# Kernel tuning notes

Measured on AMD Instinct MI355X. Metric: run time of the kernel, lower is better.

## Reference

```python
import jax, jax.numpy as jnp
import numpy as np

# dims
T, INPUT_DIM = 128, 512
C_INT, ISQ, DIM, C = 8, 16, 256, 8  # internal_channels, input_square_dim, dim, n_channel
OSQ, OUT_CH = 8, 16                  # output_square_dim, output_size // osq^2
INPUT_SCALE, S1, S2 = 1.0, 0.9, 0.1
K1, D1, K2, D2 = 3, 1, 5, 2


def dw_circ_conv(x, w, dilation):
    """Depthwise conv with circular padding. x: [B,C,H,W], w: [C,1,k,k]."""
    k = w.shape[-1]
    pad = dilation * (k - 1) // 2
    xp = jnp.pad(x, ((0, 0), (0, 0), (pad, pad), (pad, pad)), mode='wrap')
    return jax.lax.conv_general_dilated(
        xp, w, window_strides=(1, 1), padding='VALID',
        rhs_dilation=(dilation, dilation), feature_group_count=x.shape[1])


def setup_inputs() -> dict:
    key = jax.random.key(0)
    ks = jax.random.split(key, 10)
    X = jax.random.normal(ks[0], (T, INPUT_DIM), jnp.float32)
    # nn.Linear weight [out, in]
    W_embed = jax.random.normal(ks[1], (C_INT * ISQ * ISQ, INPUT_DIM), jnp.float32) * 0.02
    mask_coarse = jax.random.bernoulli(ks[2], 0.5, (1, 1, ISQ, ISQ)).astype(jnp.float32)
    mask_fine = jax.random.bernoulli(ks[3], 0.5, (1, 1, DIM, DIM)).astype(jnp.float32)
    # ConvTranspose2d weight [in_ch, out_ch, k, k], k = dim // isq = 16
    W_deconv = jax.random.normal(ks[4], (C_INT, C, DIM // ISQ, DIM // ISQ), jnp.float32) * 0.02

    def lateral_w(k, ksz, p):
        # LateralConnections with conn_exp=1: |w| * bernoulli(p), normalized per output channel
        w = jnp.abs(jax.random.normal(k, (C, 1, ksz, ksz), jnp.float32))
        m = jax.random.bernoulli(jax.random.fold_in(k, 1), p, w.shape).astype(jnp.float32)
        w = w * m
        return w / w.sum(axis=(1, 2, 3), keepdims=True)

    w1 = lateral_w(ks[5], K1, 0.9)
    w2 = lateral_w(ks[6], K2, 0.9)
    # output Conv2d: [out_ch, in_ch, k, k], k = dim // osq = 32
    w_out = jax.random.normal(ks[7], (OUT_CH, C, DIM // OSQ, DIM // OSQ), jnp.float32) * 0.01
    b_out = jax.random.normal(ks[8], (OUT_CH,), jnp.float32) * 0.01
    return dict(X=X, W_embed=W_embed, mask_coarse=mask_coarse, mask_fine=mask_fine,
                W_deconv=W_deconv, w1=w1, w2=w2, w_out=w_out, b_out=b_out)


def reference(X, W_embed, mask_coarse, mask_fine, W_deconv, w1, w2, w_out, b_out):
    t = X.shape[0]
    ksz = W_deconv.shape[-1]
    # CorticalInput
    u = (X @ W_embed.T).reshape(t, C_INT, ISQ, ISQ) * mask_coarse  # [T,Cint,isq,isq]
    # ConvTranspose2d with stride == kernel_size (non-overlapping) == block expansion
    u = jnp.einsum('tcij,coab->toiajb', u, W_deconv).reshape(t, C, ISQ * ksz, ISQ * ksz)
    u = INPUT_SCALE * u * mask_fine  # [T,C,dim,dim]

    # sequential reservoir scan
    def step(Z, x):
        Z = jnp.tanh(S1 * dw_circ_conv(Z, w1, D1) + S2 * dw_circ_conv(Z, w2, D2) + x)
        return Z, Z[0]

    Z0 = jnp.zeros((1, C, DIM, DIM), X.dtype)
    _, outs = jax.lax.scan(step, Z0, u)  # outs: [T,C,dim,dim]

    # readout conv (kernel == stride == dim // osq)
    ko = w_out.shape[-1]
    y = jax.lax.conv_general_dilated(outs, w_out, (ko, ko), 'VALID')
    y = y + b_out[None, :, None, None]
    return y.reshape(t, -1)
```

## Files before the change

### kernel.cpp

```cpp
#include <hip/hip_runtime.h>
#include <math.h>

#define SB_OFF   0
#define E_OFF    524288
#define YP_OFF   786432
#define FLAG_OFF 1835008

__device__ __forceinline__ float fast_tanh(float x) {
  x = fminf(fmaxf(x, -15.f), 15.f);
  float ex = __expf(2.f * x);
  return __fdividef(ex - 1.f, ex + 1.f);
}

__device__ __forceinline__ float2 aload_f2(const float* p) {
  unsigned long long v = __hip_atomic_load((const unsigned long long*)p,
                                           __ATOMIC_RELAXED, __HIP_MEMORY_SCOPE_AGENT);
  float2 r;
  r.x = __uint_as_float((unsigned)v);
  r.y = __uint_as_float((unsigned)(v >> 32));
  return r;
}
__device__ __forceinline__ void astore_f2(float* p, float a, float b) {
  unsigned long long v =
      ((unsigned long long)__float_as_uint(b) << 32) | (unsigned long long)__float_as_uint(a);
  __hip_atomic_store((unsigned long long*)p, v, __ATOMIC_RELAXED, __HIP_MEMORY_SCOPE_AGENT);
}

__global__ __launch_bounds__(256) void prep_kernel(
    const float* __restrict__ X, const float* __restrict__ W_embed,
    const float* __restrict__ mask_coarse, float* __restrict__ ws)
{
  const int tid = threadIdx.x, bid = blockIdx.x;
  float* eb = ws + E_OFF;
  unsigned* flags = (unsigned*)(ws + FLAG_OFF);
  if (bid < 16) flags[bid * 256 + tid] = 0;

  const int o  = bid * 16 + (tid & 15);
  const int t0 = (tid >> 4) * 8;
  const float4* Wf4 = (const float4*)W_embed + (size_t)o * 128;
  const float4* Xf4 = (const float4*)X;
  float acc[8];
#pragma unroll
  for (int i = 0; i < 8; ++i) acc[i] = 0.f;
  for (int k4 = 0; k4 < 128; ++k4) {
    float4 wv = Wf4[k4];
#pragma unroll
    for (int tt = 0; tt < 8; ++tt) {
      float4 xv = Xf4[(size_t)(t0 + tt) * 128 + k4];
      acc[tt] = fmaf(wv.x, xv.x, fmaf(wv.y, xv.y, fmaf(wv.z, xv.z, fmaf(wv.w, xv.w, acc[tt]))));
    }
  }
  float mc = mask_coarse[o & 255];
#pragma unroll
  for (int tt = 0; tt < 8; ++tt)
    eb[(size_t)(t0 + tt) * 2048 + o] = acc[tt] * mc;
}

__global__ __launch_bounds__(512, 2) void scan_kernel(
    const float* __restrict__ mask_fine, const float* __restrict__ W_deconv,
    const float* __restrict__ w1, const float* __restrict__ w2,
    const float* __restrict__ w_out, float* __restrict__ ws)
{
  __shared__ float zin[72 * 44];
  __shared__ float rowbuf[64 * 19];

  const int tid  = threadIdx.x;
  const int bid  = blockIdx.x;
  const int ch   = bid >> 5;
  const int tile = bid & 31;
  const int tI = tile >> 3, tJ = tile & 7;
  const int r0 = tI << 6, c0 = tJ << 5;
  const int row = tid >> 3;
  const int cg  = tid & 7;
  const int lc  = cg << 2;

  float* Zb = ws + SB_OFF;
  const float* eb = ws + E_OFF;
  float* yp = ws + YP_OFF;
  unsigned* flags_all = (unsigned*)(ws + FLAG_OFF);
  unsigned* myf = flags_all + bid * 16;
  const int myoff = (ch * 32 + tile) << 10;

  const int a16 = row & 15;
  const int b16 = lc & 15;
  const int i0  = (r0 + row) >> 4;
  const int jj  = (c0 + lc) >> 4;
  float4 wd[8];
#pragma unroll
  for (int c = 0; c < 8; ++c)
    wd[c] = *(const float4*)&W_deconv[(((c * 8 + ch) * 16) + a16) * 16 + b16];
  float4 mf = *(const float4*)&mask_fine[(size_t)(r0 + row) * 256 + c0 + lc];
  float4 wo[16];
#pragma unroll
  for (int oc = 0; oc < 16; ++oc)
    wo[oc] = *(const float4*)&w_out[(((oc * 8 + ch) * 32) + (row & 31)) * 32 + lc];
  float w1s[9], w2s[25];
#pragma unroll
  for (int k = 0; k < 9; ++k)
    w1s[k] = __uint_as_float(__builtin_amdgcn_readfirstlane(__float_as_uint(w1[ch * 9 + k])));
#pragma unroll
  for (int k = 0; k < 25; ++k)
    w2s[k] = __uint_as_float(__builtin_amdgcn_readfirstlane(__float_as_uint(w2[ch * 25 + k])));

  int h_soff = 0, h_dst = 0, h_nrec = 0;
  const unsigned* h_flag = nullptr;
  const bool has_halo = (tid < 416);
  {
    int u = tid, di = 0, dj = 0;
    if (u < 64) {
      int r = u >> 4, cp = (u & 15) << 1;
      di = -1; dj = 0; h_soff = 128 + r * 32 + cp; h_dst = r * 44 + 4 + cp;
    } else if (u < 128) {
      int v = u - 64; int r = v >> 4, cp = (v & 15) << 1;
      di = 1; dj = 0; h_soff = 0 + r * 32 + cp; h_dst = (68 + r) * 44 + 4 + cp;
    } else if (u < 256) {
      int v = u - 128; int r = v >> 1, c = (v & 1) << 1;
      di = 0; dj = -1; h_soff = 512 + r * 4 + c; h_dst = (4 + r) * 44 + c;
    } else if (u < 384) {
      int v = u - 256; int r = v >> 1, c = (v & 1) << 1;
      di = 0; dj = 1; h_soff = 256 + r * 4 + c; h_dst = (4 + r) * 44 + 36 + c;
    } else if (u < 416) {
      int v = u - 384; int corner = v >> 3; int k = v & 7;
      int r = k >> 1, c = (k & 1) << 1;
      if (corner == 0)      { di = -1; dj = -1; h_soff = 816 + r * 4 + c; h_dst = r * 44 + c; }
      else if (corner == 1) { di = -1; dj = 1;  h_soff = 800 + r * 4 + c; h_dst = r * 44 + 36 + c; }
      else if (corner == 2) { di = 1;  dj = -1; h_soff = 784 + r * 4 + c; h_dst = (68 + r) * 44 + c; }
      else                  { di = 1;  dj = 1;  h_soff = 768 + r * 4 + c; h_dst = (68 + r) * 44 + 36 + c; }
    }
    int nI = (tI + di) & 3, nJ = (tJ + dj) & 7;
    h_nrec = (ch * 32 + nI * 8 + nJ) << 10;
    h_flag = flags_all + (ch * 32 + nI * 8 + nJ) * 16;
  }

  for (int k = tid; k < 72 * 44; k += 512) zin[k] = 0.f;
  __syncthreads();

  for (int t = 0; t < 128; ++t) {
    float* sb = Zb + (size_t)((t + 1) & 1) * 262144;
    float* myrec = sb + myoff;

    float ev[8];
#pragma unroll
    for (int c = 0; c < 8; ++c)
      ev[c] = eb[(size_t)t * 2048 + c * 256 + i0 * 16 + jj];

    float c1a[4] = {0, 0, 0, 0}, c2a[4] = {0, 0, 0, 0};
    {
      float w[12];
      auto load_row = [&](int zr) {
        float4 A  = *(const float4*)&zin[zr * 44 + lc];
        float4 B  = *(const float4*)&zin[zr * 44 + lc + 4];
        float4 Cq = *(const float4*)&zin[zr * 44 + lc + 8];
        w[0]=A.x; w[1]=A.y; w[2]=A.z; w[3]=A.w;
        w[4]=B.x; w[5]=B.y; w[6]=B.z; w[7]=B.w;
        w[8]=Cq.x; w[9]=Cq.y; w[10]=Cq.z; w[11]=Cq.w;
      };
      auto k2row = [&](int a) {
#pragma unroll
        for (int j = 0; j < 4; ++j)
#pragma unroll
          for (int b = 0; b < 5; ++b)
            c2a[j] = fmaf(w[j + 2 * b], w2s[a * 5 + b], c2a[j]);
      };
      auto k1row = [&](int a) {
#pragma unroll
        for (int j = 0; j < 4; ++j)
#pragma unroll
          for (int b = 0; b < 3; ++b)
            c1a[j] = fmaf(w[j + 3 + b], w1s[a * 3 + b], c1a[j]);
      };
      load_row(row + 0); k2row(0);
      load_row(row + 2); k2row(1);
      load_row(row + 3); k1row(0);
      load_row(row + 4); k1row(1); k2row(2);
      load_row(row + 5); k1row(2);
      load_row(row + 6); k2row(3);
      load_row(row + 8); k2row(4);
    }
    float zv[4];
    {
      const float* mfp = (const float*)&mf;
#pragma unroll
      for (int j = 0; j < 4; ++j) {
        float u = 0.f;
#pragma unroll
        for (int c = 0; c < 8; ++c)
          u = fmaf(ev[c], ((const float*)&wd[c])[j], u);
        float val = fmaf(0.9f, c1a[j], fmaf(0.1f, c2a[j], mfp[j] * u));
        zv[j] = fast_tanh(val);
      }
    }
    float racc[16];
#pragma unroll
    for (int oc = 0; oc < 16; ++oc) {
      const float* wop = (const float*)&wo[oc];
      racc[oc] = fmaf(zv[0], wop[0], fmaf(zv[1], wop[1], fmaf(zv[2], wop[2], zv[3] * wop[3])));
    }

    __syncthreads();

    *(float4*)&zin[(4 + row) * 44 + 4 + lc] = make_float4(zv[0], zv[1], zv[2], zv[3]);
    if (row < 4) {
      float* p = myrec + 0 + row * 32 + lc;
      astore_f2(p, zv[0], zv[1]); astore_f2(p + 2, zv[2], zv[3]);
    }
    if (row >= 60) {
      float* p = myrec + 128 + (row - 60) * 32 + lc;
      astore_f2(p, zv[0], zv[1]); astore_f2(p + 2, zv[2], zv[3]);
    }
    if (lc == 0) {
      float* p = myrec + 256 + row * 4;
      astore_f2(p, zv[0], zv[1]); astore_f2(p + 2, zv[2], zv[3]);
    }
    if (lc == 28) {
      float* p = myrec + 512 + row * 4;
      astore_f2(p, zv[0], zv[1]); astore_f2(p + 2, zv[2], zv[3]);
    }
    if (row < 4 && lc == 0) {
      float* p = myrec + 768 + row * 4;
      astore_f2(p, zv[0], zv[1]); astore_f2(p + 2, zv[2], zv[3]);
    }
    if (row < 4 && lc == 28) {
      float* p = myrec + 784 + row * 4;
      astore_f2(p, zv[0], zv[1]); astore_f2(p + 2, zv[2], zv[3]);
    }
    if (row >= 60 && lc == 0) {
      float* p = myrec + 800 + (row - 60) * 4;
      astore_f2(p, zv[0], zv[1]); astore_f2(p + 2, zv[2], zv[3]);
    }
    if (row >= 60 && lc == 28) {
      float* p = myrec + 816 + (row - 60) * 4;
      astore_f2(p, zv[0], zv[1]); astore_f2(p + 2, zv[2], zv[3]);
    }

    __syncthreads();

    if (t < 127 && tid == 0)
      __hip_atomic_store(myf, (unsigned)(t + 1), __ATOMIC_RELAXED, __HIP_MEMORY_SCOPE_AGENT);

#pragma unroll
    for (int m = 1; m <= 4; m <<= 1)
#pragma unroll
      for (int k = 0; k < 16; ++k)
        racc[k] += __shfl_xor(racc[k], m, 64);
    rowbuf[row * 19 + (cg << 1)]     = racc[cg << 1];
    rowbuf[row * 19 + (cg << 1) + 1] = racc[(cg << 1) + 1];

    if (t < 127 && has_halo) {
      int spins = 0;
      while (__hip_atomic_load(h_flag, __ATOMIC_RELAXED, __HIP_MEMORY_SCOPE_AGENT) <
             (unsigned)(t + 1)) {
        __builtin_amdgcn_s_sleep(1);
        if (++spins > (1 << 20)) break;
      }
      float2 v2 = aload_f2(sb + h_nrec + h_soff);
      *(float2*)&zin[h_dst] = v2;
    }

    __syncthreads();

    if (tid < 32) {
      int p = tid >> 4, oc = tid & 15;
      float s = 0.f;
#pragma unroll
      for (int r = 0; r < 32; ++r) s += rowbuf[(p * 32 + r) * 19 + oc];
      yp[(((size_t)ch * 64 + (2 * tI + p) * 8 + tJ) * 128 + t) * 16 + oc] = s;
    }
  }
}

__global__ __launch_bounds__(256) void final_kernel(
    const float* __restrict__ b_out, const float* __restrict__ ws, float* __restrict__ out)
{
  int idx = blockIdx.x * 256 + threadIdx.x;
  int t = idx >> 10;
  int rem = idx & 1023;
  int oc = rem >> 6;
  int IJ = rem & 63;
  const float* yp = ws + YP_OFF;
  float s = b_out[oc];
#pragma unroll
  for (int c = 0; c < 8; ++c)
    s += yp[(((size_t)c * 64 + IJ) * 128 + t) * 16 + oc];
  out[idx] = s;
}

extern "C" void kernel_launch(void* const* d_in, const int* in_sizes, int n_in,
                              void* d_out, int out_size, void* d_ws, size_t ws_size,
                              hipStream_t stream) {
  const float* X           = (const float*)d_in[0];
  const float* W_embed     = (const float*)d_in[1];
  const float* mask_coarse = (const float*)d_in[2];
  const float* mask_fine   = (const float*)d_in[3];
  const float* W_deconv    = (const float*)d_in[4];
  const float* w1          = (const float*)d_in[5];
  const float* w2          = (const float*)d_in[6];
  const float* w_out       = (const float*)d_in[7];
  const float* b_out       = (const float*)d_in[8];
  float* ws  = (float*)d_ws;
  float* out = (float*)d_out;

  prep_kernel<<<dim3(128), dim3(256), 0, stream>>>(X, W_embed, mask_coarse, ws);
  scan_kernel<<<dim3(256), dim3(512), 0, stream>>>(mask_fine, W_deconv, w1, w2, w_out, ws);
  final_kernel<<<dim3(512), dim3(256), 0, stream>>>(b_out, ws, out);
}
```

Measured before the change: 589.7 us.

## Replace per-block halo flags with value-tagged halo records

Each halo value is now stored together with a timestep tag in a single 64-bit atomic store, so neighbours poll the data word directly instead of waiting on a separate per-block flag. This removes one __syncthreads and the flag publish from each timestep, and halo stores are issued earlier, right after tanh. The cost is doubled halo record size, more store and load instructions, and two polling loads per thread for some threads. The prep kernel is also reshaped to 256 blocks with 4 timesteps per thread, and the flag-zeroing step is dropped.

```diff
diff --git a/kernel.cpp b/kernel.cpp
--- a/kernel.cpp
+++ b/kernel.cpp
@@ -2,9 +2,8 @@
 #include <math.h>
 
 #define SB_OFF   0
-#define E_OFF    524288
-#define YP_OFF   786432
-#define FLAG_OFF 1835008
+#define E_OFF    1048576
+#define YP_OFF   1310720
 
 __device__ __forceinline__ float fast_tanh(float x) {
   x = fminf(fmaxf(x, -15.f), 15.f);
@@ -32,27 +31,22 @@
 {
   const int tid = threadIdx.x, bid = blockIdx.x;
   float* eb = ws + E_OFF;
-  unsigned* flags = (unsigned*)(ws + FLAG_OFF);
-  if (bid < 16) flags[bid * 256 + tid] = 0;
-
-  const int o  = bid * 16 + (tid & 15);
-  const int t0 = (tid >> 4) * 8;
+  const int o  = bid * 8 + (tid >> 5);
+  const int t0 = (tid & 31) * 4;
   const float4* Wf4 = (const float4*)W_embed + (size_t)o * 128;
   const float4* Xf4 = (const float4*)X;
-  float acc[8];
-#pragma unroll
-  for (int i = 0; i < 8; ++i) acc[i] = 0.f;
+  float acc[4] = {0.f, 0.f, 0.f, 0.f};
   for (int k4 = 0; k4 < 128; ++k4) {
     float4 wv = Wf4[k4];
 #pragma unroll
-    for (int tt = 0; tt < 8; ++tt) {
+    for (int tt = 0; tt < 4; ++tt) {
       float4 xv = Xf4[(size_t)(t0 + tt) * 128 + k4];
       acc[tt] = fmaf(wv.x, xv.x, fmaf(wv.y, xv.y, fmaf(wv.z, xv.z, fmaf(wv.w, xv.w, acc[tt]))));
     }
   }
   float mc = mask_coarse[o & 255];
 #pragma unroll
-  for (int tt = 0; tt < 8; ++tt)
+  for (int tt = 0; tt < 4; ++tt)
     eb[(size_t)(t0 + tt) * 2048 + o] = acc[tt] * mc;
 }
 
@@ -77,9 +71,7 @@
   float* Zb = ws + SB_OFF;
   const float* eb = ws + E_OFF;
   float* yp = ws + YP_OFF;
-  unsigned* flags_all = (unsigned*)(ws + FLAG_OFF);
-  unsigned* myf = flags_all + bid * 16;
-  const int myoff = (ch * 32 + tile) << 10;
+  const int myoff = (ch * 32 + tile) << 11;
 
   const int a16 = row & 15;
   const int b16 = lc & 15;
@@ -102,42 +94,45 @@
   for (int k = 0; k < 25; ++k)
     w2s[k] = __uint_as_float(__builtin_amdgcn_readfirstlane(__float_as_uint(w2[ch * 25 + k])));
 
-  int h_soff = 0, h_dst = 0, h_nrec = 0;
-  const unsigned* h_flag = nullptr;
-  const bool has_halo = (tid < 416);
+  int rd_off[2] = {0, 0}, rd_dst[2] = {0, 0};
   {
-    int u = tid, di = 0, dj = 0;
-    if (u < 64) {
-      int r = u >> 4, cp = (u & 15) << 1;
-      di = -1; dj = 0; h_soff = 128 + r * 32 + cp; h_dst = r * 44 + 4 + cp;
-    } else if (u < 128) {
-      int v = u - 64; int r = v >> 4, cp = (v & 15) << 1;
-      di = 1; dj = 0; h_soff = 0 + r * 32 + cp; h_dst = (68 + r) * 44 + 4 + cp;
-    } else if (u < 256) {
-      int v = u - 128; int r = v >> 1, c = (v & 1) << 1;
-      di = 0; dj = -1; h_soff = 512 + r * 4 + c; h_dst = (4 + r) * 44 + c;
-    } else if (u < 384) {
-      int v = u - 256; int r = v >> 1, c = (v & 1) << 1;
-      di = 0; dj = 1; h_soff = 256 + r * 4 + c; h_dst = (4 + r) * 44 + 36 + c;
-    } else if (u < 416) {
-      int v = u - 384; int corner = v >> 3; int k = v & 7;
-      int r = k >> 1, c = (k & 1) << 1;
-      if (corner == 0)      { di = -1; dj = -1; h_soff = 816 + r * 4 + c; h_dst = r * 44 + c; }
-      else if (corner == 1) { di = -1; dj = 1;  h_soff = 800 + r * 4 + c; h_dst = r * 44 + 36 + c; }
-      else if (corner == 2) { di = 1;  dj = -1; h_soff = 784 + r * 4 + c; h_dst = (68 + r) * 44 + c; }
-      else                  { di = 1;  dj = 1;  h_soff = 768 + r * 4 + c; h_dst = (68 + r) * 44 + 36 + c; }
-    }
-    int nI = (tI + di) & 3, nJ = (tJ + dj) & 7;
-    h_nrec = (ch * 32 + nI * 8 + nJ) << 10;
-    h_flag = flags_all + (ch * 32 + nI * 8 + nJ) * 16;
+    int n = 0;
+    auto setup = [&](int u) {
+      int di = 0, dj = 0, off = 0, dst = 0;
+      if (u < 128) {
+        int r = u >> 5, c = u & 31;
+        di = -1; dj = 0; off = 256 + 2 * u; dst = r * 44 + 4 + c;
+      } else if (u < 256) {
+        int v = u - 128;
+        di = 1; dj = 0; off = 2 * v; dst = (68 + (v >> 5)) * 44 + 4 + (v & 31);
+      } else if (u < 512) {
+        int v = u - 256;
+        di = 0; dj = -1; off = 1024 + 2 * v; dst = (4 + (v >> 2)) * 44 + (v & 3);
+      } else if (u < 768) {
+        int v = u - 512;
+        di = 0; dj = 1; off = 512 + 2 * v; dst = (4 + (v >> 2)) * 44 + 36 + (v & 3);
+      } else {
+        int v = u - 768; int corner = v >> 4, k = v & 15, r = k >> 2, c = k & 3;
+        if (corner == 0)      { di = -1; dj = -1; off = 1632 + 2 * k; dst = r * 44 + c; }
+        else if (corner == 1) { di = -1; dj = 1;  off = 1600 + 2 * k; dst = r * 44 + 36 + c; }
+        else if (corner == 2) { di = 1;  dj = -1; off = 1568 + 2 * k; dst = (68 + r) * 44 + c; }
+        else                  { di = 1;  dj = 1;  off = 1536 + 2 * k; dst = (68 + r) * 44 + 36 + c; }
+      }
+      int nI = (tI + di) & 3, nJ = (tJ + dj) & 7;
+      rd_off[n] = ((ch * 32 + nI * 8 + nJ) << 11) + off;
+      rd_dst[n] = dst;
+      ++n;
+    };
+    setup(tid);
+    if (tid < 320) setup(tid + 512);
   }
+  const bool has2 = (tid < 320);
 
   for (int k = tid; k < 72 * 44; k += 512) zin[k] = 0.f;
   __syncthreads();
 
   for (int t = 0; t < 128; ++t) {
-    float* sb = Zb + (size_t)((t + 1) & 1) * 262144;
-    float* myrec = sb + myoff;
+    float* sb = Zb + (size_t)((t + 1) & 1) * 524288;
 
     float ev[8];
 #pragma unroll
@@ -190,6 +185,52 @@
         zv[j] = fast_tanh(val);
       }
     }
+
+    if (t < 127) {
+      float* myrec = sb + myoff;
+      const float tagf = __uint_as_float((unsigned)(t + 1));
+      if (row < 4) {
+#pragma unroll
+        for (int j = 0; j < 4; ++j)
+          astore_f2(myrec + 2 * (row * 32 + lc + j), zv[j], tagf);
+      }
+      if (row >= 60) {
+#pragma unroll
+        for (int j = 0; j < 4; ++j)
+          astore_f2(myrec + 256 + 2 * ((row - 60) * 32 + lc + j), zv[j], tagf);
+      }
+      if (lc == 0) {
+#pragma unroll
+        for (int j = 0; j < 4; ++j)
+          astore_f2(myrec + 512 + 2 * (row * 4 + j), zv[j], tagf);
+      }
+      if (lc == 28) {
+#pragma unroll
+        for (int j = 0; j < 4; ++j)
+          astore_f2(myrec + 1024 + 2 * (row * 4 + j), zv[j], tagf);
+      }
+      if (row < 4 && lc == 0) {
+#pragma unroll
+        for (int j = 0; j < 4; ++j)
+          astore_f2(myrec + 1536 + 2 * (row * 4 + j), zv[j], tagf);
+      }
+      if (row < 4 && lc == 28) {
+#pragma unroll
+        for (int j = 0; j < 4; ++j)
+          astore_f2(myrec + 1568 + 2 * (row * 4 + j), zv[j], tagf);
+      }
+      if (row >= 60 && lc == 0) {
+#pragma unroll
+        for (int j = 0; j < 4; ++j)
+          astore_f2(myrec + 1600 + 2 * ((row - 60) * 4 + j), zv[j], tagf);
+      }
+      if (row >= 60 && lc == 28) {
+#pragma unroll
+        for (int j = 0; j < 4; ++j)
+          astore_f2(myrec + 1632 + 2 * ((row - 60) * 4 + j), zv[j], tagf);
+      }
+    }
+
     float racc[16];
 #pragma unroll
     for (int oc = 0; oc < 16; ++oc) {
@@ -200,43 +241,6 @@
     __syncthreads();
 
     *(float4*)&zin[(4 + row) * 44 + 4 + lc] = make_float4(zv[0], zv[1], zv[2], zv[3]);
-    if (row < 4) {
-      float* p = myrec + 0 + row * 32 + lc;
-      astore_f2(p, zv[0], zv[1]); astore_f2(p + 2, zv[2], zv[3]);
-    }
-    if (row >= 60) {
-      float* p = myrec + 128 + (row - 60) * 32 + lc;
-      astore_f2(p, zv[0], zv[1]); astore_f2(p + 2, zv[2], zv[3]);
-    }
-    if (lc == 0) {
-      float* p = myrec + 256 + row * 4;
-      astore_f2(p, zv[0], zv[1]); astore_f2(p + 2, zv[2], zv[3]);
-    }
-    if (lc == 28) {
-      float* p = myrec + 512 + row * 4;
-      astore_f2(p, zv[0], zv[1]); astore_f2(p + 2, zv[2], zv[3]);
-    }
-    if (row < 4 && lc == 0) {
-      float* p = myrec + 768 + row * 4;
-      astore_f2(p, zv[0], zv[1]); astore_f2(p + 2, zv[2], zv[3]);
-    }
-    if (row < 4 && lc == 28) {
-      float* p = myrec + 784 + row * 4;
-      astore_f2(p, zv[0], zv[1]); astore_f2(p + 2, zv[2], zv[3]);
-    }
-    if (row >= 60 && lc == 0) {
-      float* p = myrec + 800 + (row - 60) * 4;
-      astore_f2(p, zv[0], zv[1]); astore_f2(p + 2, zv[2], zv[3]);
-    }
-    if (row >= 60 && lc == 28) {
-      float* p = myrec + 816 + (row - 60) * 4;
-      astore_f2(p, zv[0], zv[1]); astore_f2(p + 2, zv[2], zv[3]);
-    }
-
-    __syncthreads();
-
-    if (t < 127 && tid == 0)
-      __hip_atomic_store(myf, (unsigned)(t + 1), __ATOMIC_RELAXED, __HIP_MEMORY_SCOPE_AGENT);
 
 #pragma unroll
     for (int m = 1; m <= 4; m <<= 1)
@@ -246,15 +250,26 @@
     rowbuf[row * 19 + (cg << 1)]     = racc[cg << 1];
     rowbuf[row * 19 + (cg << 1) + 1] = racc[(cg << 1) + 1];
 
-    if (t < 127 && has_halo) {
-      int spins = 0;
-      while (__hip_atomic_load(h_flag, __ATOMIC_RELAXED, __HIP_MEMORY_SCOPE_AGENT) <
-             (unsigned)(t + 1)) {
-        __builtin_amdgcn_s_sleep(1);
-        if (++spins > (1 << 20)) break;
-      }
-      float2 v2 = aload_f2(sb + h_nrec + h_soff);
-      *(float2*)&zin[h_dst] = v2;
+    if (t < 127) {
+      const unsigned tg = (unsigned)(t + 1);
+      {
+        const float* p = sb + rd_off[0];
+        float2 v2; int spins = 0;
+        do { v2 = aload_f2(p);
+             if (__float_as_uint(v2.y) == tg) break;
+             __builtin_amdgcn_s_sleep(1);
+        } while (++spins < (1 << 17));
+        zin[rd_dst[0]] = v2.x;
+      }
+      if (has2) {
+        const float* p = sb + rd_off[1];
+        float2 v2; int spins = 0;
+        do { v2 = aload_f2(p);
+             if (__float_as_uint(v2.y) == tg) break;
+             __builtin_amdgcn_s_sleep(1);
+        } while (++spins < (1 << 17));
+        zin[rd_dst[1]] = v2.x;
+      }
     }
 
     __syncthreads();
@@ -300,7 +315,7 @@
   float* ws  = (float*)d_ws;
   float* out = (float*)d_out;
 
-  prep_kernel<<<dim3(128), dim3(256), 0, stream>>>(X, W_embed, mask_coarse, ws);
+  prep_kernel<<<dim3(256), dim3(256), 0, stream>>>(X, W_embed, mask_coarse, ws);
   scan_kernel<<<dim3(256), dim3(512), 0, stream>>>(mask_fine, W_deconv, w1, w2, w_out, ws);
   final_kernel<<<dim3(512), dim3(256), 0, stream>>>(b_out, ws, out);
 }
```

After: 595.8 us. Within noise of the previous version (+1.0%).
